# Kernel optimization log

Measured on AMD Instinct MI355X. Metric: run time of the kernel, lower is better.

## Reference

```python
import jax, jax.numpy as jnp
import numpy as np

NUM_EMBEDDINGS = 1024
EMBEDDING_DIM = 256


def setup_inputs() -> dict:
    key = jax.random.key(0)
    k1, k2 = jax.random.split(key)
    x = jax.random.normal(k1, (64, EMBEDDING_DIM, 32, 32), dtype=jnp.float32)
    # torch.nn.init.uniform_ default is U[0,1)
    embeddings = jax.random.uniform(k2, (EMBEDDING_DIM, NUM_EMBEDDINGS), dtype=jnp.float32)
    return {"x": x, "embeddings": embeddings}


def reference(x, embeddings):
    # x: [B, C, H, W] with C == embedding_dim; embeddings: [D, K]
    B, C, H, W = x.shape
    x_perm = jnp.transpose(x, (0, 2, 3, 1))           # [B, H, W, D]
    flat = x_perm.reshape(-1, C)                      # [N, D]
    sim = flat @ embeddings                           # [N, K] GEMM
    dists = (jnp.sum(flat * flat, axis=1, keepdims=True)
             + jnp.sum(embeddings * embeddings, axis=0)
             - 2.0 * sim)                             # [N, K]
    indices = jnp.argmin(dists, axis=1)               # [N]
    # one-hot @ embeddings.T is just a row gather of embeddings.T
    quantized = embeddings.T[indices]                 # [N, D]
    quantized = quantized.reshape(x_perm.shape)       # [B, H, W, D]
    # straight-through estimator
    q_ste = x_perm + jax.lax.stop_gradient(quantized - x_perm)
    q_ste = jnp.transpose(q_ste, (0, 3, 1, 2))        # [B, C, H, W]
    quantized = jnp.transpose(quantized, (0, 3, 1, 2))
    return q_ste, quantized, indices
```

## Files before the change

kernel.cpp:

```cpp
#include <hip/hip_runtime.h>

typedef unsigned short u16;
typedef unsigned int   u32;

#define DCH  256
#define KCB  1024
#define HW   1024
#define NPOS 65536
#define MARGIN 0.07f

#define ESQ_WS   0
#define IDX_WS   4096
#define FCNT_WS  266240
#define FLIST_WS 266304
#define ESQD_WS  528448ull
#define XH_WS    1048576ull
#define EH_WS    34603008ull

using f32x4 = __attribute__((ext_vector_type(4))) float;
using f16x8 = __attribute__((ext_vector_type(8))) _Float16;

__device__ __forceinline__ u16 f2h(float x) {
    _Float16 h = (_Float16)x;
    return *reinterpret_cast<u16*>(&h);
}

__device__ __forceinline__ void gl_lds16(const void* g, void* l) {
    __builtin_amdgcn_global_load_lds(
        (const __attribute__((address_space(1))) void*)g,
        (__attribute__((address_space(3))) void*)l, 16, 0, 0);
}

__device__ __forceinline__ void transpose_slice(const float* __restrict__ src,
                                                u16* __restrict__ dst,
                                                int b, int pc, int cc, int tid) {
    __shared__ float Xs[32][260];
    const int p0 = pc * 256;
    const int c0 = cc * 32;
    const size_t nbase = (size_t)b * 1024 + p0;
#pragma unroll
    for (int r = 0; r < 8; ++r) {
        int id4 = tid + 256 * r;
        int c = id4 >> 6;
        int q = id4 & 63;
        float4 v = *reinterpret_cast<const float4*>(
            src + (size_t)b * 262144 + (size_t)(c0 + c) * 1024 + p0 + q * 4);
        *reinterpret_cast<float4*>(&Xs[c][q * 4]) = v;
    }
    __syncthreads();
    const int p = tid;
#pragma unroll
    for (int dg = 0; dg < 4; ++dg) {
        u32 w0, w1, w2, w3;
        {
            float f0 = Xs[dg * 8 + 0][p], f1 = Xs[dg * 8 + 1][p];
            float f2 = Xs[dg * 8 + 2][p], f3 = Xs[dg * 8 + 3][p];
            float f4 = Xs[dg * 8 + 4][p], f5 = Xs[dg * 8 + 5][p];
            float f6 = Xs[dg * 8 + 6][p], f7 = Xs[dg * 8 + 7][p];
            w0 = (u32)f2h(f0) | ((u32)f2h(f1) << 16);
            w1 = (u32)f2h(f2) | ((u32)f2h(f3) << 16);
            w2 = (u32)f2h(f4) | ((u32)f2h(f5) << 16);
            w3 = (u32)f2h(f6) | ((u32)f2h(f7) << 16);
        }
        uint4 ov = {w0, w1, w2, w3};
        *reinterpret_cast<uint4*>(dst + (nbase + p) * 256 + c0 + dg * 8) = ov;
    }
}

__global__ __launch_bounds__(256) void prep_all(const float* __restrict__ X,
                                                const float* __restrict__ E,
                                                u16* __restrict__ Xh,
                                                u16* __restrict__ Eh,
                                                float* __restrict__ esq,
                                                double* __restrict__ esqd,
                                                int* __restrict__ fcnt) {
    const int tid = threadIdx.x;
    const int bid = blockIdx.x;
    if (bid < 2048) {
        transpose_slice(X, Xh, bid >> 5, (bid >> 3) & 3, bid & 7, tid);
    } else if (bid < 2080) {
        int b2 = bid - 2048;
        transpose_slice(E, Eh, 0, (b2 >> 3) & 3, b2 & 7, tid);
    } else {
        if (bid == 2080 && tid == 0) *fcnt = 0;
        int k = (bid - 2080) * 256 + tid;
        double s = 0.0;
#pragma unroll 8
        for (int c = 0; c < DCH; ++c) {
            double e = (double)E[c * KCB + k];
            s = fma(e, e, s);
        }
        esq[k] = (float)s;
        esqd[k] = s;
    }
}

#define BUFS  32768
#define EB_O  16384
#define ESQ_O 65536
#define MRG_O 69632
#define SM_SZ 72704

__global__ __launch_bounds__(256, 2) void vq_main_mfma(
        const u16* __restrict__ XhG, const u16* __restrict__ EhG,
        const float* __restrict__ esq,
        int* __restrict__ idx_out, int* __restrict__ flag_cnt,
        int* __restrict__ flag_list) {
    __shared__ alignas(16) char sm[SM_SZ];
    const int tid = threadIdx.x;
    const int l = tid & 63;
    const int w = tid >> 6;
    const int wm = w >> 1, wn = w & 1;
    const int pbase = blockIdx.x * 128;

    *reinterpret_cast<float4*>(sm + ESQ_O + tid * 16) =
        *reinterpret_cast<const float4*>(esq + tid * 4);

    const int srow = w * 32 + (l >> 3);
    const int sswz = ((l & 7) ^ (l >> 3)) * 16;
    const char* XhB = reinterpret_cast<const char*>(XhG);
    const char* EhB = reinterpret_cast<const char*>(EhG);
    const size_t xbase = (size_t)(pbase + srow) * 512 + sswz;
    const size_t ebase = (size_t)srow * 512 + sswz;

    const int sA0 = (((l >> 4) ^ (l & 7))) * 16;
    const int addrA0 = wm * 8192 + (l & 15) * 128 + sA0;
    const int addrB0 = wn * 8192 + (l & 15) * 128 + sA0;

    auto STAGE = [&](int bufo, int nt, int kt) {
        const size_t xo = xbase + (size_t)kt * 128;
        const size_t eo = ebase + (size_t)nt * 65536 + (size_t)kt * 128;
#pragma unroll
        for (int k = 0; k < 4; ++k) {
            gl_lds16(XhB + xo + k * 4096, sm + bufo + (w * 4 + k) * 1024);
            gl_lds16(EhB + eo + k * 4096, sm + bufo + EB_O + (w * 4 + k) * 1024);
        }
    };

    float b1[16], b2[16];
    int   i1[16];
#pragma unroll
    for (int q = 0; q < 16; ++q) { b1[q] = 3.4e38f; b2[q] = 3.4e38f; i1[q] = 0; }

    STAGE(0, 0, 0);
    __syncthreads();

    int step = 0;
    for (int nt = 0; nt < 8; ++nt) {
        f32x4 acc[4][4];
#pragma unroll
        for (int i = 0; i < 4; ++i)
#pragma unroll
            for (int j = 0; j < 4; ++j)
#pragma unroll
                for (int r = 0; r < 4; ++r) acc[i][j][r] = 0.f;

        for (int kt = 0; kt < 4; ++kt) {
            int nxt = step + 1;
            if (nxt < 32) STAGE((nxt & 1) * BUFS, nxt >> 2, nxt & 3);
            const char* bo = sm + (step & 1) * BUFS;
#pragma unroll
            for (int ds = 0; ds < 2; ++ds) {
                const int so = ds * 64;
                f16x8 a[4], bh[4];
#pragma unroll
                for (int i = 0; i < 4; ++i)
                    a[i] = *reinterpret_cast<const f16x8*>(bo + ((addrA0 ^ so) + i * 2048));
#pragma unroll
                for (int j = 0; j < 4; ++j)
                    bh[j] = *reinterpret_cast<const f16x8*>(bo + EB_O + ((addrB0 ^ so) + j * 2048));
#pragma unroll
                for (int i = 0; i < 4; ++i)
#pragma unroll
                    for (int j = 0; j < 4; ++j)
                        acc[i][j] = __builtin_amdgcn_mfma_f32_16x16x32_f16(a[i], bh[j], acc[i][j], 0, 0, 0);
            }
            __syncthreads();
            ++step;
        }

        const int kb = nt * 128 + wn * 64 + (l & 15);
        float eq[4];
#pragma unroll
        for (int j = 0; j < 4; ++j)
            eq[j] = *reinterpret_cast<const float*>(sm + ESQ_O + (kb + j * 16) * 4);
#pragma unroll
        for (int i = 0; i < 4; ++i)
#pragma unroll
            for (int j = 0; j < 4; ++j)
#pragma unroll
                for (int r = 0; r < 4; ++r) {
                    float s = fmaf(-2.f, acc[i][j][r], eq[j]);
                    int ri = i * 4 + r;
                    bool lt = s < b1[ri];
                    b2[ri] = fminf(b2[ri], fmaxf(s, b1[ri]));
                    i1[ri] = lt ? (kb + j * 16) : i1[ri];
                    b1[ri] = fminf(b1[ri], s);
                }
    }

#pragma unroll
    for (int m = 1; m <= 8; m <<= 1) {
#pragma unroll
        for (int q = 0; q < 16; ++q) {
            float ob1 = __shfl_xor(b1[q], m);
            float ob2 = __shfl_xor(b2[q], m);
            int   oi  = __shfl_xor(i1[q], m);
            bool lt = ob1 < b1[q];
            b2[q] = fminf(fminf(b2[q], ob2), fmaxf(b1[q], ob1));
            i1[q] = lt ? oi : i1[q];
            b1[q] = fminf(b1[q], ob1);
        }
    }

    if ((l & 15) == 0) {
#pragma unroll
        for (int i = 0; i < 4; ++i)
#pragma unroll
            for (int r = 0; r < 4; ++r) {
                int q = i * 4 + r;
                int rl = wm * 64 + i * 16 + (l >> 4) * 4 + r;
                *reinterpret_cast<float*>(sm + MRG_O + (rl * 2 + wn) * 4) = b1[q];
                *reinterpret_cast<float*>(sm + MRG_O + 1024 + (rl * 2 + wn) * 4) = b2[q];
                *reinterpret_cast<int*>(sm + MRG_O + 2048 + (rl * 2 + wn) * 4) = i1[q];
            }
    }
    __syncthreads();
    if (tid < 128) {
        float a1 = *reinterpret_cast<float*>(sm + MRG_O + (tid * 2 + 0) * 4);
        float a2 = *reinterpret_cast<float*>(sm + MRG_O + 1024 + (tid * 2 + 0) * 4);
        int   ai = *reinterpret_cast<int*>(sm + MRG_O + 2048 + (tid * 2 + 0) * 4);
        float c1 = *reinterpret_cast<float*>(sm + MRG_O + (tid * 2 + 1) * 4);
        float c2 = *reinterpret_cast<float*>(sm + MRG_O + 1024 + (tid * 2 + 1) * 4);
        int   ci = *reinterpret_cast<int*>(sm + MRG_O + 2048 + (tid * 2 + 1) * 4);
        bool lt = c1 < a1;
        float B1 = fminf(a1, c1);
        float B2 = fminf(fminf(a2, c2), fmaxf(a1, c1));
        int I1 = lt ? ci : ai;
        int n = pbase + tid;
        idx_out[n] = I1;
        if (B2 - B1 < MARGIN) {
            int s2 = atomicAdd(flag_cnt, 1);
            flag_list[s2] = n;
        }
    }
}

#define RFPB 2
__global__ __launch_bounds__(256) void vq_repair(const float* __restrict__ X,
                                                 const float* __restrict__ E,
                                                 const double* __restrict__ esqd,
                                                 int* __restrict__ idx_out,
                                                 const int* __restrict__ flag_cnt,
                                                 const int* __restrict__ flag_list) {
    __shared__ double xs[RFPB][256];
    __shared__ double rd[RFPB][256];
    __shared__ int    ri[RFPB][256];
    const int tid = threadIdx.x;
    const int cnt = *flag_cnt;
    for (int f0 = blockIdx.x * RFPB; f0 < cnt; f0 += gridDim.x * RFPB) {
#pragma unroll
        for (int g = 0; g < RFPB; ++g) {
            int f = f0 + g;
            int n = flag_list[f < cnt ? f : f0];
            int b = n >> 10, p = n & 1023;
            xs[g][tid] = (double)X[(size_t)b * 262144 + (size_t)tid * 1024 + p];
        }
        __syncthreads();
        double s[RFPB][4];
#pragma unroll
        for (int g = 0; g < RFPB; ++g)
#pragma unroll
            for (int j = 0; j < 4; ++j) s[g][j] = 0.0;
        const float4* Erow = reinterpret_cast<const float4*>(E) + tid;
#pragma unroll 2
        for (int c = 0; c < 256; ++c) {
            float4 ev = Erow[c * 256];
            double e0 = (double)ev.x, e1 = (double)ev.y, e2 = (double)ev.z, e3 = (double)ev.w;
#pragma unroll
            for (int g = 0; g < RFPB; ++g) {
                double xv = xs[g][c];
                s[g][0] = fma(xv, e0, s[g][0]);
                s[g][1] = fma(xv, e1, s[g][1]);
                s[g][2] = fma(xv, e2, s[g][2]);
                s[g][3] = fma(xv, e3, s[g][3]);
            }
        }
        const int k0 = tid * 4;
        const double eq0 = esqd[k0], eq1 = esqd[k0 + 1], eq2 = esqd[k0 + 2], eq3 = esqd[k0 + 3];
#pragma unroll
        for (int g = 0; g < RFPB; ++g) {
            double d0 = eq0 - 2.0 * s[g][0];
            double d1 = eq1 - 2.0 * s[g][1];
            double d2 = eq2 - 2.0 * s[g][2];
            double d3 = eq3 - 2.0 * s[g][3];
            double bd = d0; int bi = k0;
            if (d1 < bd) { bd = d1; bi = k0 + 1; }
            if (d2 < bd) { bd = d2; bi = k0 + 2; }
            if (d3 < bd) { bd = d3; bi = k0 + 3; }
            rd[g][tid] = bd; ri[g][tid] = bi;
        }
        __syncthreads();
        for (int off = 128; off > 0; off >>= 1) {
            if (tid < off) {
#pragma unroll
                for (int g = 0; g < RFPB; ++g) {
                    double od = rd[g][tid + off]; int oi = ri[g][tid + off];
                    if (od < rd[g][tid] || (od == rd[g][tid] && oi < ri[g][tid])) {
                        rd[g][tid] = od; ri[g][tid] = oi;
                    }
                }
            }
            __syncthreads();
        }
        if (tid < RFPB && (f0 + tid) < cnt) {
            idx_out[flag_list[f0 + tid]] = ri[tid][0];
        }
        __syncthreads();
    }
}

#define WCC 8
__global__ __launch_bounds__(256) void vq_write(const float* __restrict__ E,
                                                const int* __restrict__ idx_ws,
                                                float* __restrict__ out0,
                                                float* __restrict__ out1,
                                                float* __restrict__ out2) {
    __shared__ float Es[WCC][1024];
    const int tid = threadIdx.x;
    const int b   = blockIdx.x >> 5;
    const int cch = blockIdx.x & 31;
#pragma unroll
    for (int r = 0; r < 8; ++r) {
        int id4 = tid + 256 * r;
        int c = id4 >> 8;
        int q = id4 & 255;
        *reinterpret_cast<float4*>(&Es[c][q * 4]) =
            *reinterpret_cast<const float4*>(E + (size_t)(cch * WCC + c) * 1024 + q * 4);
    }
    int4 kv = *reinterpret_cast<const int4*>(idx_ws + b * 1024 + tid * 4);
    __syncthreads();
    if (cch == 0) {
        float4 v = {(float)kv.x, (float)kv.y, (float)kv.z, (float)kv.w};
        *reinterpret_cast<float4*>(out2 + b * 1024 + tid * 4) = v;
    }
#pragma unroll
    for (int c = 0; c < WCC; ++c) {
        f32x4 v = {Es[c][kv.x], Es[c][kv.y], Es[c][kv.z], Es[c][kv.w]};
        size_t o = (size_t)b * 262144 + (size_t)(cch * WCC + c) * 1024 + tid * 4;
        __builtin_nontemporal_store(v, reinterpret_cast<f32x4*>(out0 + o));
        __builtin_nontemporal_store(v, reinterpret_cast<f32x4*>(out1 + o));
    }
}

extern "C" void kernel_launch(void* const* d_in, const int* in_sizes, int n_in,
                              void* d_out, int out_size, void* d_ws, size_t ws_size,
                              hipStream_t stream) {
    const float* X = (const float*)d_in[0];
    const float* E = (const float*)d_in[1];
    float* out = (float*)d_out;
    char* ws = (char*)d_ws;

    float* esq   = (float*)(ws + ESQ_WS);
    int* idx     = (int*)(ws + IDX_WS);
    int* fcnt    = (int*)(ws + FCNT_WS);
    int* flist   = (int*)(ws + FLIST_WS);
    double* esqd = (double*)(ws + ESQD_WS);
    u16* Xh      = (u16*)(ws + XH_WS);
    u16* Eh      = (u16*)(ws + EH_WS);

    prep_all<<<2084, 256, 0, stream>>>(X, E, Xh, Eh, esq, esqd, fcnt);
    vq_main_mfma<<<512, 256, 0, stream>>>(Xh, Eh, esq, idx, fcnt, flist);
    vq_repair<<<2048, 256, 0, stream>>>(X, E, esqd, idx, fcnt, flist);
    vq_write<<<2048, 256, 0, stream>>>(E, idx,
                                       out,
                                       out + 16777216,
                                       out + 33554432);
}
```

Measured before the change: 153.3 us.

## Fuse X transpose and fp16 conversion into main MFMA kernel, keeping X tile in registers

Removes the separate pass that transposed all of X to an fp16 workspace buffer. Instead, each main-kernel block loads its 128-position float32 slice of X through LDS, converts it to fp16 and holds it in registers, then writes it into the swizzled LDS buffer at each k-step. Only E tiles are still streamed from global memory. This saves the global write and re-read of the 32 MB fp16 X copy, but adds 64 registers per thread. The launch bound of 2 blocks per SM is dropped, so occupancy may fall.

```diff
diff --git a/kernel.cpp b/kernel.cpp
--- a/kernel.cpp
+++ b/kernel.cpp
@@ -14,11 +14,11 @@
 #define FCNT_WS  266240
 #define FLIST_WS 266304
 #define ESQD_WS  528448ull
-#define XH_WS    1048576ull
-#define EH_WS    34603008ull
+#define EH_WS    1048576ull
 
 using f32x4 = __attribute__((ext_vector_type(4))) float;
 using f16x8 = __attribute__((ext_vector_type(8))) _Float16;
+using u32x4 = __attribute__((ext_vector_type(4))) u32;
 
 __device__ __forceinline__ u16 f2h(float x) {
     _Float16 h = (_Float16)x;
@@ -67,23 +67,18 @@
     }
 }
 
-__global__ __launch_bounds__(256) void prep_all(const float* __restrict__ X,
-                                                const float* __restrict__ E,
-                                                u16* __restrict__ Xh,
+__global__ __launch_bounds__(256) void prep_all(const float* __restrict__ E,
                                                 u16* __restrict__ Eh,
                                                 float* __restrict__ esq,
                                                 double* __restrict__ esqd,
                                                 int* __restrict__ fcnt) {
     const int tid = threadIdx.x;
     const int bid = blockIdx.x;
-    if (bid < 2048) {
-        transpose_slice(X, Xh, bid >> 5, (bid >> 3) & 3, bid & 7, tid);
-    } else if (bid < 2080) {
-        int b2 = bid - 2048;
-        transpose_slice(E, Eh, 0, (b2 >> 3) & 3, b2 & 7, tid);
+    if (bid < 32) {
+        transpose_slice(E, Eh, 0, bid >> 3, bid & 7, tid);
     } else {
-        if (bid == 2080 && tid == 0) *fcnt = 0;
-        int k = (bid - 2080) * 256 + tid;
+        if (bid == 32 && tid == 0) *fcnt = 0;
+        int k = (bid - 32) * 256 + tid;
         double s = 0.0;
 #pragma unroll 8
         for (int c = 0; c < DCH; ++c) {
@@ -101,8 +96,8 @@
 #define MRG_O 69632
 #define SM_SZ 72704
 
-__global__ __launch_bounds__(256, 2) void vq_main_mfma(
-        const u16* __restrict__ XhG, const u16* __restrict__ EhG,
+__global__ __launch_bounds__(256) void vq_main_mfma(
+        const float* __restrict__ X, const u16* __restrict__ EhG,
         const float* __restrict__ esq,
         int* __restrict__ idx_out, int* __restrict__ flag_cnt,
         int* __restrict__ flag_list) {
@@ -116,34 +111,98 @@
     *reinterpret_cast<float4*>(sm + ESQ_O + tid * 16) =
         *reinterpret_cast<const float4*>(esq + tid * 4);
 
+    const int tp  = tid & 127;
+    const int thi = tid >> 7;
+    u32x4 xr[4][4];
+    {
+        const float* Xb = X + (size_t)(pbase >> 10) * 262144 + (pbase & 1023);
+#pragma unroll
+        for (int kt = 0; kt < 4; ++kt) {
+#pragma unroll
+            for (int r = 0; r < 8; ++r) {
+                int g = r * 256 + tid;
+                gl_lds16(Xb + (size_t)(kt * 64 + (g >> 5)) * 1024 + (size_t)(g & 31) * 4,
+                         sm + g * 16);
+            }
+            __syncthreads();
+#pragma unroll
+            for (int s = 0; s < 4; ++s) {
+                int c = thi * 4 + s;
+#pragma unroll
+                for (int m = 0; m < 4; ++m) {
+                    float x0 = *reinterpret_cast<const float*>(sm + (c * 8 + m * 2 + 0) * 512 + tp * 4);
+                    float x1 = *reinterpret_cast<const float*>(sm + (c * 8 + m * 2 + 1) * 512 + tp * 4);
+                    xr[kt][s][m] = (u32)f2h(x0) | ((u32)f2h(x1) << 16);
+                }
+            }
+            __syncthreads();
+        }
+    }
+    const int xw0 = tp * 128 + (((thi * 4 + 0) ^ (tp & 7)) * 16);
+    const int xw1 = tp * 128 + (((thi * 4 + 1) ^ (tp & 7)) * 16);
+    const int xw2 = tp * 128 + (((thi * 4 + 2) ^ (tp & 7)) * 16);
+    const int xw3 = tp * 128 + (((thi * 4 + 3) ^ (tp & 7)) * 16);
+
     const int srow = w * 32 + (l >> 3);
     const int sswz = ((l & 7) ^ (l >> 3)) * 16;
-    const char* XhB = reinterpret_cast<const char*>(XhG);
     const char* EhB = reinterpret_cast<const char*>(EhG);
-    const size_t xbase = (size_t)(pbase + srow) * 512 + sswz;
     const size_t ebase = (size_t)srow * 512 + sswz;
 
     const int sA0 = (((l >> 4) ^ (l & 7))) * 16;
     const int addrA0 = wm * 8192 + (l & 15) * 128 + sA0;
     const int addrB0 = wn * 8192 + (l & 15) * 128 + sA0;
 
-    auto STAGE = [&](int bufo, int nt, int kt) {
-        const size_t xo = xbase + (size_t)kt * 128;
-        const size_t eo = ebase + (size_t)nt * 65536 + (size_t)kt * 128;
-#pragma unroll
-        for (int k = 0; k < 4; ++k) {
-            gl_lds16(XhB + xo + k * 4096, sm + bufo + (w * 4 + k) * 1024);
-            gl_lds16(EhB + eo + k * 4096, sm + bufo + EB_O + (w * 4 + k) * 1024);
-        }
-    };
-
     float b1[16], b2[16];
     int   i1[16];
 #pragma unroll
     for (int q = 0; q < 16; ++q) { b1[q] = 3.4e38f; b2[q] = 3.4e38f; i1[q] = 0; }
 
-    STAGE(0, 0, 0);
+    {
+        *reinterpret_cast<u32x4*>(sm + xw0) = xr[0][0];
+        *reinterpret_cast<u32x4*>(sm + xw1) = xr[0][1];
+        *reinterpret_cast<u32x4*>(sm + xw2) = xr[0][2];
+        *reinterpret_cast<u32x4*>(sm + xw3) = xr[0][3];
+#pragma unroll
+        for (int k = 0; k < 4; ++k)
+            gl_lds16(EhB + ebase + k * 4096, sm + EB_O + (w * 4 + k) * 1024);
+    }
     __syncthreads();
+
+#define KSTEP(NKT)                                                              \
+    {                                                                           \
+        int nxt = step + 1;                                                     \
+        if (nxt < 32) {                                                         \
+            int bufo = (nxt & 1) * BUFS;                                        \
+            *reinterpret_cast<u32x4*>(sm + bufo + xw0) = xr[NKT][0];            \
+            *reinterpret_cast<u32x4*>(sm + bufo + xw1) = xr[NKT][1];            \
+            *reinterpret_cast<u32x4*>(sm + bufo + xw2) = xr[NKT][2];            \
+            *reinterpret_cast<u32x4*>(sm + bufo + xw3) = xr[NKT][3];            \
+            const size_t eo = ebase + (size_t)(nxt >> 2) * 65536 + (size_t)(NKT) * 128; \
+            gl_lds16(EhB + eo,         sm + bufo + EB_O + (w * 4 + 0) * 1024);  \
+            gl_lds16(EhB + eo +  4096, sm + bufo + EB_O + (w * 4 + 1) * 1024);  \
+            gl_lds16(EhB + eo +  8192, sm + bufo + EB_O + (w * 4 + 2) * 1024);  \
+            gl_lds16(EhB + eo + 12288, sm + bufo + EB_O + (w * 4 + 3) * 1024);  \
+        }                                                                       \
+        const char* bo = sm + (step & 1) * BUFS;                                \
+        _Pragma("unroll")                                                       \
+        for (int ds = 0; ds < 2; ++ds) {                                        \
+            const int so = ds * 64;                                             \
+            f16x8 a[4], bh[4];                                                  \
+            _Pragma("unroll")                                                   \
+            for (int i = 0; i < 4; ++i)                                         \
+                a[i] = *reinterpret_cast<const f16x8*>(bo + ((addrA0 ^ so) + i * 2048)); \
+            _Pragma("unroll")                                                   \
+            for (int j = 0; j < 4; ++j)                                         \
+                bh[j] = *reinterpret_cast<const f16x8*>(bo + EB_O + ((addrB0 ^ so) + j * 2048)); \
+            _Pragma("unroll")                                                   \
+            for (int i = 0; i < 4; ++i)                                         \
+                _Pragma("unroll")                                               \
+                for (int j = 0; j < 4; ++j)                                     \
+                    acc[i][j] = __builtin_amdgcn_mfma_f32_16x16x32_f16(a[i], bh[j], acc[i][j], 0, 0, 0); \
+        }                                                                       \
+        __syncthreads();                                                        \
+        ++step;                                                                 \
+    }
 
     int step = 0;
     for (int nt = 0; nt < 8; ++nt) {
@@ -155,29 +214,10 @@
 #pragma unroll
                 for (int r = 0; r < 4; ++r) acc[i][j][r] = 0.f;
 
-        for (int kt = 0; kt < 4; ++kt) {
-            int nxt = step + 1;
-            if (nxt < 32) STAGE((nxt & 1) * BUFS, nxt >> 2, nxt & 3);
-            const char* bo = sm + (step & 1) * BUFS;
-#pragma unroll
-            for (int ds = 0; ds < 2; ++ds) {
-                const int so = ds * 64;
-                f16x8 a[4], bh[4];
-#pragma unroll
-                for (int i = 0; i < 4; ++i)
-                    a[i] = *reinterpret_cast<const f16x8*>(bo + ((addrA0 ^ so) + i * 2048));
-#pragma unroll
-                for (int j = 0; j < 4; ++j)
-                    bh[j] = *reinterpret_cast<const f16x8*>(bo + EB_O + ((addrB0 ^ so) + j * 2048));
-#pragma unroll
-                for (int i = 0; i < 4; ++i)
-#pragma unroll
-                    for (int j = 0; j < 4; ++j)
-                        acc[i][j] = __builtin_amdgcn_mfma_f32_16x16x32_f16(a[i], bh[j], acc[i][j], 0, 0, 0);
-            }
-            __syncthreads();
-            ++step;
-        }
+        KSTEP(1)
+        KSTEP(2)
+        KSTEP(3)
+        KSTEP(0)
 
         const int kb = nt * 128 + wn * 64 + (l & 15);
         float eq[4];
@@ -198,6 +238,7 @@
                     b1[ri] = fminf(b1[ri], s);
                 }
     }
+#undef KSTEP
 
 #pragma unroll
     for (int m = 1; m <= 8; m <<= 1) {
@@ -366,11 +407,10 @@
     int* fcnt    = (int*)(ws + FCNT_WS);
     int* flist   = (int*)(ws + FLIST_WS);
     double* esqd = (double*)(ws + ESQD_WS);
-    u16* Xh      = (u16*)(ws + XH_WS);
     u16* Eh      = (u16*)(ws + EH_WS);
 
-    prep_all<<<2084, 256, 0, stream>>>(X, E, Xh, Eh, esq, esqd, fcnt);
-    vq_main_mfma<<<512, 256, 0, stream>>>(Xh, Eh, esq, idx, fcnt, flist);
+    prep_all<<<36, 256, 0, stream>>>(E, Eh, esq, esqd, fcnt);
+    vq_main_mfma<<<512, 256, 0, stream>>>(X, Eh, esq, idx, fcnt, flist);
     vq_repair<<<2048, 256, 0, stream>>>(X, E, esqd, idx, fcnt, flist);
     vq_write<<<2048, 256, 0, stream>>>(E, idx,
                                        out,
```

After: 155.0 us. About the same (+1.1%).
